# Optimization experiments

Hardware: AMD Instinct MI355X
Metric: run time of the kernel (lower is better)

Reference implementation:

```python
import jax, jax.numpy as jnp
import numpy as np

DIM = 512   # feature channels (dim)
K = 3       # depthwise kernel size
H = 256     # grid extent along pos[:,0]
W = 256     # grid extent along pos[:,1]
N = 20000   # number of occupied spots (unique coordinates)


def setup_inputs() -> dict:
    key = jax.random.key(0)
    k1, k2, k3 = jax.random.split(key, 3)
    rng = np.random.default_rng(0)
    # N unique flat cells; pin corners so the dense grid extent is exactly HxW
    flat = np.concatenate([[0, H * W - 1], rng.permutation(H * W - 2)[: N - 2] + 1])
    pos = jnp.asarray(np.stack([flat // W, flat % W], axis=1), dtype=jnp.int32)  # (N,2)
    x = jax.random.normal(k1, (1, N, DIM), jnp.float32)
    weight = jax.random.normal(k2, (DIM, 1, K, K), jnp.float32) * 0.05  # depthwise OIHW
    bias = jax.random.normal(k3, (DIM,), jnp.float32) * 0.05
    return {"x": x, "pos": pos, "weight": weight, "bias": bias}


def reference(x, pos, weight, bias):
    pos = pos - pos.min(axis=0)                 # shift to origin (as torch)
    p0, p1 = pos[:, 0], pos[:, 1]
    xsq = x[0]                                  # (N, DIM)
    # scatter sparse coords to dense grid (duplicates would sum, coords unique)
    grid = jnp.zeros((H, W, DIM), x.dtype).at[p0, p1].add(xsq)   # (H, W, DIM)
    xd = grid.transpose(2, 1, 0)[None]          # (1, DIM, W, H) == permute(2,1,0).unsqueeze(0)
    conv = jax.lax.conv_general_dilated(
        xd, weight, (1, 1), "SAME",
        dimension_numbers=("NCHW", "OIHW", "NCHW"),
        feature_group_count=DIM,
    ) + bias[None, :, None, None]
    mask = xd.sum(axis=1, keepdims=True) != 0.0  # occupied cells
    out_d = jnp.where(mask, conv, 0.0) + xd      # masked residual
    dense = out_d[0].transpose(2, 1, 0)          # (H, W, DIM)
    # gather back to sparse values; torch to_sparse(2) orders rows lexicographically
    order = jnp.lexsort((p1, p0))
    vals = dense[p0[order], p1[order]]           # (N, DIM)
    return vals[None]                            # (1, N, DIM)
```

## Files before the change

kernel.cpp:

```cpp
#include <hip/hip_runtime.h>

#define HH 256
#define WW 256
#define DIM 512

typedef float f32x4 __attribute__((ext_vector_type(4)));


__global__ __launch_bounds__(256) void scatter_kernel(const int* __restrict__ pos,
                                                      int* __restrict__ cell_map,
                                                      float* __restrict__ zrow,
                                                      int n) {
    int i = blockIdx.x * 256 + threadIdx.x;
    if (i < 512) zrow[i] = 0.0f;
    if (i >= n) return;
    int p0 = pos[2 * i];
    int p1 = pos[2 * i + 1];
    cell_map[p0 * WW + p1] = i;
}

__global__ __launch_bounds__(256) void rank_kernel(const int* __restrict__ cell_map,
                                                   int* __restrict__ sorted) {
    __shared__ int red[256];
    __shared__ int wt[4];
    const int t = threadIdx.x;
    const int b = blockIdx.x;
    const int limit = b * 256;

    int cnt = 0;
    const int4* cm4 = (const int4*)cell_map;
    for (int i = t; i * 4 < limit; i += 256) {
        int4 v = cm4[i];
        cnt += (v.x >= 0) + (v.y >= 0) + (v.z >= 0) + (v.w >= 0);
    }
    red[t] = cnt;
    __syncthreads();
    #pragma unroll
    for (int d = 128; d > 0; d >>= 1) {
        if (t < d) red[t] += red[t + d];
        __syncthreads();
    }
    int blk_off = red[0];

    int cell = limit + t;
    int m = cell_map[cell];
    bool occ = (m >= 0);
    unsigned long long mask = __ballot(occ);
    int lane = t & 63;
    int wave = t >> 6;
    int pre = __popcll(mask & ((1ull << lane) - 1ull));
    if (lane == 0) wt[wave] = __popcll(mask);
    __syncthreads();
    int woff = 0;
    for (int i = 0; i < wave; ++i) woff += wt[i];
    if (occ) sorted[blk_off + woff + pre] = (m << 16) | cell;
}

__global__ __launch_bounds__(256, 4) void conv_main(const float* __restrict__ x,
                                                    const float* __restrict__ weight,
                                                    const float* __restrict__ bias,
                                                    const int* __restrict__ cell_map,
                                                    const int* __restrict__ sorted,
                                                    const float* __restrict__ zrow,
                                                    float* __restrict__ out,
                                                    int n) {
    __shared__ float s_w[9 * DIM];
    const int t = threadIdx.x;
    for (int cc = t; cc < DIM; cc += 256) {
        const float* wp = weight + cc * 9;
        #pragma unroll
        for (int k = 0; k < 9; ++k)
            s_w[k * DIM + cc] = wp[k] + (k == 4 ? 1.0f : 0.0f);
    }
    __syncthreads();

    const int lane = t & 63;
    const int wv   = t >> 6;
    const int c0   = (wv & 1) * 256 + lane * 4;
    const int eng  = wv >> 1;

    float b0, b1, b2, b3;
    { float4 bv = *(const float4*)(bias + c0); b0 = bv.x; b1 = bv.y; b2 = bv.z; b3 = bv.w; }

    const int nb  = gridDim.x;
    const int cid = (blockIdx.x & 7) * (nb >> 3) + (blockIdx.x >> 3);
    const int ppb = (n + nb - 1) / nb;
    const int base = cid * ppb;
    int endr = base + ppb; if (endr > n) endr = n;

    int r = base + eng;
    if (r >= endr) return;
    int pk = __builtin_amdgcn_readfirstlane(sorted[r]);

    while (r < endr) {
        const int rn = r + 2;
        int pk_next = 0;
        if (rn < endr)
            pk_next = __builtin_amdgcn_readfirstlane(sorted[rn]);

        const int p    = pk >> 16;
        const int flat = pk & 0xFFFF;
        const int h = flat >> 8;
        const int w = flat & (WW - 1);

        const float* xp[9];
        #pragma unroll
        for (int k = 0; k < 9; ++k) {
            int v;
            if (k == 4) {
                v = p;
            } else {
                int dh = k % 3 - 1;
                int dw = k / 3 - 1;
                int hh = h + dh;
                int ww2 = w + dw;
                v = -1;
                if ((unsigned)hh < (unsigned)HH && (unsigned)ww2 < (unsigned)WW)
                    v = cell_map[hh * WW + ww2];
                v = __builtin_amdgcn_readfirstlane(v);
            }
            xp[k] = (v >= 0) ? (x + (size_t)v * DIM + c0) : (zrow + c0);
        }

        f32x4 x0, x1, x2, x3, x4, x5, x6, x7, x8;
        asm volatile(
            "global_load_dwordx4 %0, %9,  off\n\t"
            "global_load_dwordx4 %1, %10, off\n\t"
            "global_load_dwordx4 %2, %11, off\n\t"
            "global_load_dwordx4 %3, %12, off\n\t"
            "global_load_dwordx4 %4, %13, off\n\t"
            "global_load_dwordx4 %5, %14, off\n\t"
            "global_load_dwordx4 %6, %15, off\n\t"
            "global_load_dwordx4 %7, %16, off\n\t"
            "global_load_dwordx4 %8, %17, off\n\t"
            "s_waitcnt vmcnt(0)"
            : "=&v"(x0), "=&v"(x1), "=&v"(x2), "=&v"(x3), "=&v"(x4),
              "=&v"(x5), "=&v"(x6), "=&v"(x7), "=&v"(x8)
            : "v"(xp[0]), "v"(xp[1]), "v"(xp[2]), "v"(xp[3]), "v"(xp[4]),
              "v"(xp[5]), "v"(xp[6]), "v"(xp[7]), "v"(xp[8]));

        float a0 = b0, a1 = b1, a2 = b2, a3 = b3;
        f32x4 xv[9] = { x0, x1, x2, x3, x4, x5, x6, x7, x8 };
        #pragma unroll
        for (int k = 0; k < 9; ++k) {
            const float4 wkv = *(const float4*)(s_w + k * DIM + c0);
            a0 += xv[k].x * wkv.x;
            a1 += xv[k].y * wkv.y;
            a2 += xv[k].z * wkv.z;
            a3 += xv[k].w * wkv.w;
        }

        float* op = out + (size_t)r * DIM + c0;
        f32x4 o = { a0, a1, a2, a3 };
        __builtin_nontemporal_store(o, (f32x4*)op);

        r = rn;
        pk = pk_next;
    }
}

extern "C" void kernel_launch(void* const* d_in, const int* in_sizes, int n_in,
                              void* d_out, int out_size, void* d_ws, size_t ws_size,
                              hipStream_t stream) {
    const float* x      = (const float*)d_in[0];
    const int*   pos    = (const int*)d_in[1];
    const float* weight = (const float*)d_in[2];
    const float* bias   = (const float*)d_in[3];
    float* out = (float*)d_out;

    int n = in_sizes[1] / 2;

    int*   ws       = (int*)d_ws;
    int*   cell_map = ws;
    int*   sorted   = ws + HH * WW;
    float* zrow     = (float*)(ws + HH * WW + 20480);

    scatter_kernel<<<(n + 255) / 256, 256, 0, stream>>>(pos, cell_map, zrow, n);
    rank_kernel<<<256, 256, 0, stream>>>(cell_map, sorted);

    const int nblocks = 2048;
    conv_main<<<nblocks, 256, 0, stream>>>(x, weight, bias, cell_map, sorted, zrow, out, n);
}
```

Baseline: 134.4 us.

## Prefetch neighbor cell_map lookups one iteration ahead using per-lane gather

Replaces the eight serial scalar-uniform cell_map loads per output row with one vector gather in which lane k loads neighbor k, then broadcasts each value with readlane. Both the neighbor lookup and the sorted-index read are software-pipelined: indices two rows ahead and neighbor maps one row ahead are fetched while the current row computes. This is meant to hide the dependent-load latency chain that precedes the nine feature loads. In exchange it adds register pressure and clamped out-of-range addressing, with the validity check moved to after the load.

```diff
diff --git a/kernel.cpp b/kernel.cpp
--- a/kernel.cpp
+++ b/kernel.cpp
@@ -82,6 +82,10 @@
     float b0, b1, b2, b3;
     { float4 bv = *(const float4*)(bias + c0); b0 = bv.x; b1 = bv.y; b2 = bv.z; b3 = bv.w; }
 
+    const int kk  = lane < 9 ? lane : 8;
+    const int pdh = kk % 3 - 1;
+    const int pdw = kk / 3 - 1;
+
     const int nb  = gridDim.x;
     const int cid = (blockIdx.x & 7) * (nb >> 3) + (blockIdx.x >> 3);
     const int ppb = (n + nb - 1) / nb;
@@ -90,18 +94,33 @@
 
     int r = base + eng;
     if (r >= endr) return;
-    int pk = __builtin_amdgcn_readfirstlane(sorted[r]);
+
+    int pk_cur = __builtin_amdgcn_readfirstlane(sorted[r]);
+    int pv_cur;
+    {
+        int h = (pk_cur & 0xFFFF) >> 8;
+        int w = pk_cur & (WW - 1);
+        int hh = h + pdh; hh = hh < 0 ? 0 : (hh > HH - 1 ? HH - 1 : hh);
+        int ww2 = w + pdw; ww2 = ww2 < 0 ? 0 : (ww2 > WW - 1 ? WW - 1 : ww2);
+        pv_cur = cell_map[hh * WW + ww2];
+    }
+    int pk_nxt = (r + 2 < endr) ? __builtin_amdgcn_readfirstlane(sorted[r + 2]) : 0;
 
     while (r < endr) {
-        const int rn = r + 2;
-        int pk_next = 0;
-        if (rn < endr)
-            pk_next = __builtin_amdgcn_readfirstlane(sorted[rn]);
-
-        const int p    = pk >> 16;
-        const int flat = pk & 0xFFFF;
+        const int p    = pk_cur >> 16;
+        const int flat = pk_cur & 0xFFFF;
         const int h = flat >> 8;
         const int w = flat & (WW - 1);
+
+        int pv_nxt = -1;
+        if (r + 2 < endr) {
+            int hn = (pk_nxt & 0xFFFF) >> 8;
+            int wn = pk_nxt & (WW - 1);
+            int hh = hn + pdh; hh = hh < 0 ? 0 : (hh > HH - 1 ? HH - 1 : hh);
+            int ww2 = wn + pdw; ww2 = ww2 < 0 ? 0 : (ww2 > WW - 1 ? WW - 1 : ww2);
+            pv_nxt = cell_map[hh * WW + ww2];
+        }
+        int pk_nxt2 = (r + 4 < endr) ? __builtin_amdgcn_readfirstlane(sorted[r + 4]) : 0;
 
         const float* xp[9];
         #pragma unroll
@@ -112,12 +131,10 @@
             } else {
                 int dh = k % 3 - 1;
                 int dw = k / 3 - 1;
-                int hh = h + dh;
-                int ww2 = w + dw;
-                v = -1;
-                if ((unsigned)hh < (unsigned)HH && (unsigned)ww2 < (unsigned)WW)
-                    v = cell_map[hh * WW + ww2];
-                v = __builtin_amdgcn_readfirstlane(v);
+                int vr = __builtin_amdgcn_readlane(pv_cur, k);
+                bool ok = ((unsigned)(h + dh) < (unsigned)HH) &&
+                          ((unsigned)(w + dw) < (unsigned)WW);
+                v = ok ? vr : -1;
             }
             xp[k] = (v >= 0) ? (x + (size_t)v * DIM + c0) : (zrow + c0);
         }
@@ -154,8 +171,10 @@
         f32x4 o = { a0, a1, a2, a3 };
         __builtin_nontemporal_store(o, (f32x4*)op);
 
-        r = rn;
-        pk = pk_next;
+        r += 2;
+        pk_cur = pk_nxt;
+        pk_nxt = pk_nxt2;
+        pv_cur = pv_nxt;
     }
 }
 
```

Measured after the change: 124.0 us. -7.7%, faster.
